# Kernel tuning notes

Hardware: AMD Instinct MI355X
Metric: run time of the kernel (lower is better)

Reference implementation:

```python
import jax, jax.numpy as jnp
import numpy as np

TEMPERATURE = 0.5
EPS = 1e-8  # matches torch cosine_similarity eps guard semantics (norm clamp)


def setup_inputs() -> dict:
    key = jax.random.key(0)
    k1, k2 = jax.random.split(key)
    B, D = 4096, 256
    z_i = jax.random.normal(k1, (B, D), dtype=jnp.float32)
    z_j = jax.random.normal(k2, (B, D), dtype=jnp.float32)
    return {"z_i": z_i, "z_j": z_j}


def reference(z_i, z_j):
    B = z_i.shape[0]
    z = jnp.concatenate([z_i, z_j], axis=0)            # [2B, D]
    # cosine similarity: normalize once, then GEMM
    norm = jnp.maximum(jnp.linalg.norm(z, axis=1, keepdims=True), EPS)
    zn = z / norm                                       # [2B, D]
    sim = zn @ zn.T                                     # [2B, 2B]
    # positives: diag(sim, +B) and diag(sim, -B)
    idx = jnp.arange(B)
    sim_ij = sim[idx, idx + B]
    sim_ji = sim[idx + B, idx]
    positives = jnp.concatenate([sim_ij, sim_ji])       # [2B]
    # masked denominator: exclude self-similarity
    mask = 1.0 - jnp.eye(2 * B, dtype=sim.dtype)
    denom = jnp.sum(mask * jnp.exp(sim / TEMPERATURE), axis=1)  # [2B]
    all_losses = -jnp.log(jnp.exp(positives / TEMPERATURE) / denom)
    return jnp.sum(all_losses) / (2 * B)
```

## Files before the change

kernel.cpp:

```cpp
#include <hip/hip_runtime.h>
#include <hip/hip_bf16.h>
#include <cstdint>
#include <cstddef>
#include <math.h>

#define D 256
#define TEMP_INV 2.0f
#define EPS_NORM 1e-8f
#define NTILES 2080

typedef __attribute__((ext_vector_type(8))) short bf16x8;
typedef __attribute__((ext_vector_type(4))) float f32x4;

__global__ void __launch_bounds__(256) normalize_rows(
    const float* __restrict__ zi, const float* __restrict__ zj,
    __hip_bfloat16* __restrict__ zn, float* __restrict__ denom, int B) {
  const int wid = threadIdx.x >> 6;
  const int lane = threadIdx.x & 63;
  if (threadIdx.x < 16) denom[blockIdx.x * 16 + threadIdx.x] = 0.0f;
#pragma unroll
  for (int it = 0; it < 4; ++it) {
    int row = it * 2048 + blockIdx.x * 4 + wid;
    const float* src = (row < B) ? (zi + (size_t)row * D)
                                 : (zj + (size_t)(row - B) * D);
    float4 v = ((const float4*)src)[lane];
    float ss = v.x * v.x + v.y * v.y + v.z * v.z + v.w * v.w;
    for (int off = 32; off; off >>= 1) ss += __shfl_xor(ss, off);
    float rn = 1.0f / fmaxf(sqrtf(ss), EPS_NORM);
    union { ushort4 u; __hip_bfloat16 h[4]; } o;
    o.h[0] = __float2bfloat16(v.x * rn);
    o.h[1] = __float2bfloat16(v.y * rn);
    o.h[2] = __float2bfloat16(v.z * rn);
    o.h[3] = __float2bfloat16(v.w * rn);
    ((ushort4*)zn)[(size_t)row * (D / 4) + lane] = o.u;
  }
}

__device__ __forceinline__ void decode_tile(int t, int Nb, int& by, int& bx) {
  float fb = (2.0f * Nb + 1.0f -
              sqrtf((float)((2 * Nb + 1) * (2 * Nb + 1) - 8 * t))) * 0.5f;
  int y = (int)fb;
  while ((y + 1) * Nb - ((y + 1) * y) / 2 <= t) ++y;
  while (y * Nb - (y * (y - 1)) / 2 > t) --y;
  by = y;
  bx = y + (t - (y * Nb - (y * (y - 1)) / 2));
}

__global__ void ntxent_gemm(
    const __hip_bfloat16* __restrict__ zn,
    float* __restrict__ denom, float* __restrict__ pos, int B) {
  __shared__ __align__(16) __hip_bfloat16 Ash[128 * 64];
  __shared__ __align__(16) __hip_bfloat16 Bsh[128 * 64];

  const int Nb = (2 * B) / 128;
  int by, bx;
  decode_tile(blockIdx.x, Nb, by, bx);
  const int bm = by * 128;
  const int bn = bx * 128;
  const bool isDiag = (by == bx);
  const bool isPos = (bx == by + B / 128);

  const int tid = threadIdx.x;
  const int wid = tid >> 6;
  const int lane = tid & 63;
  const int wy = wid >> 1, wx = wid & 1;
  const int wrow0 = wid * 32;

  const int lr = lane >> 3;
  const int c8 = lane & 7;

  const int frow = lane & 15;
  const int quad = lane >> 4;
  const int f7 = frow & 7;

  f32x4 acc[4][4] = {};

  const __hip_bfloat16* gA = zn + (size_t)(bm + wrow0 + lr) * D + c8 * 8;
  const __hip_bfloat16* gB = zn + (size_t)(bn + wrow0 + lr) * D + c8 * 8;
  const int ldsoff = (wrow0 + lr) * 64 + (c8 ^ lr) * 8;

#pragma unroll
  for (int k0i = 0; k0i < 4; ++k0i) {
    const int k0 = k0i * 64;
    float4 va0 = *(const float4*)(gA + 0 * 8 * D + k0);
    float4 va1 = *(const float4*)(gA + 1 * 8 * D + k0);
    float4 va2 = *(const float4*)(gA + 2 * 8 * D + k0);
    float4 va3 = *(const float4*)(gA + 3 * 8 * D + k0);
    float4 vb0 = *(const float4*)(gB + 0 * 8 * D + k0);
    float4 vb1 = *(const float4*)(gB + 1 * 8 * D + k0);
    float4 vb2 = *(const float4*)(gB + 2 * 8 * D + k0);
    float4 vb3 = *(const float4*)(gB + 3 * 8 * D + k0);
    __syncthreads();
    *(float4*)&Ash[ldsoff + 0 * 8 * 64] = va0;
    *(float4*)&Ash[ldsoff + 1 * 8 * 64] = va1;
    *(float4*)&Ash[ldsoff + 2 * 8 * 64] = va2;
    *(float4*)&Ash[ldsoff + 3 * 8 * 64] = va3;
    *(float4*)&Bsh[ldsoff + 0 * 8 * 64] = vb0;
    *(float4*)&Bsh[ldsoff + 1 * 8 * 64] = vb1;
    *(float4*)&Bsh[ldsoff + 2 * 8 * 64] = vb2;
    *(float4*)&Bsh[ldsoff + 3 * 8 * 64] = vb3;
    __syncthreads();
#pragma unroll
    for (int kk = 0; kk < 2; ++kk) {
      bf16x8 a[4], b[4];
#pragma unroll
      for (int i = 0; i < 4; ++i)
        a[i] = *(const bf16x8*)
            &Ash[(wy * 64 + i * 16 + frow) * 64 + ((kk * 4 + quad) ^ f7) * 8];
#pragma unroll
      for (int j = 0; j < 4; ++j)
        b[j] = *(const bf16x8*)
            &Bsh[(wx * 64 + j * 16 + frow) * 64 + ((kk * 4 + quad) ^ f7) * 8];
#pragma unroll
      for (int i = 0; i < 4; ++i)
#pragma unroll
        for (int j = 0; j < 4; ++j)
          acc[i][j] =
              __builtin_amdgcn_mfma_f32_16x16x32_bf16(a[i], b[j], acc[i][j], 0, 0, 0);
    }
  }

  const int colq = lane & 15;
  float cs[4] = {0.0f, 0.0f, 0.0f, 0.0f};
#pragma unroll
  for (int i = 0; i < 4; ++i) {
#pragma unroll
    for (int r = 0; r < 4; ++r) {
      int row = bm + wy * 64 + i * 16 + quad * 4 + r;
      float rs = 0.0f;
#pragma unroll
      for (int j = 0; j < 4; ++j) {
        int col = bn + wx * 64 + j * 16 + colq;
        float v = acc[i][j][r];
        float e = __expf(v * TEMP_INV);
        e = (isDiag && col == row) ? 0.0f : e;
        rs += e;
        cs[j] += e;
        if (isPos && col == row + B) { pos[row] = v; pos[col] = v; }
      }
      rs += __shfl_xor(rs, 1);
      rs += __shfl_xor(rs, 2);
      rs += __shfl_xor(rs, 4);
      rs += __shfl_xor(rs, 8);
      if (colq == 0) atomicAdd(&denom[row], rs);
    }
  }
  if (!isDiag) {
#pragma unroll
    for (int j = 0; j < 4; ++j) {
      float c = cs[j];
      c += __shfl_xor(c, 16);
      c += __shfl_xor(c, 32);
      if (quad == 0) atomicAdd(&denom[bn + wx * 64 + j * 16 + colq], c);
    }
  }
}

__global__ void __launch_bounds__(1024) finalize(
    const float* __restrict__ denom, const float* __restrict__ pos,
    float* __restrict__ out, int N) {
  __shared__ float red[16];
  const int tid = threadIdx.x;
  float s = 0.0f;
  for (int i = tid; i < N / 4; i += 1024) {
    float4 d = ((const float4*)denom)[i];
    float4 p = ((const float4*)pos)[i];
    s += __logf(d.x) - p.x * TEMP_INV;
    s += __logf(d.y) - p.y * TEMP_INV;
    s += __logf(d.z) - p.z * TEMP_INV;
    s += __logf(d.w) - p.w * TEMP_INV;
  }
  for (int off = 32; off; off >>= 1) s += __shfl_xor(s, off);
  if ((tid & 63) == 0) red[tid >> 6] = s;
  __syncthreads();
  if (tid < 16) {
    s = red[tid];
    s += __shfl_xor(s, 1);
    s += __shfl_xor(s, 2);
    s += __shfl_xor(s, 4);
    s += __shfl_xor(s, 8);
    if (tid == 0) out[0] = s / (float)N;
  }
}

extern "C" void kernel_launch(void* const* d_in, const int* in_sizes, int n_in,
                              void* d_out, int out_size, void* d_ws, size_t ws_size,
                              hipStream_t stream) {
  const float* zi = (const float*)d_in[0];
  const float* zj = (const float*)d_in[1];
  const int B = in_sizes[0] / D;
  const int N = 2 * B;

  __hip_bfloat16* zn = (__hip_bfloat16*)d_ws;
  float* denom = (float*)((char*)d_ws + (size_t)N * D * sizeof(__hip_bfloat16));
  float* pos = denom + N;

  normalize_rows<<<512, 256, 0, stream>>>(zi, zj, zn, denom, B);
  ntxent_gemm<<<NTILES, 256, 0, stream>>>(zn, denom, pos, B);
  finalize<<<1, 1024, 0, stream>>>(denom, pos, (float*)d_out, N);
}
```

Baseline: 107.9 us.

## Use 256x128 supertiles and fuse finalize into GEMM via ticket counter

The GEMM now processes 256x128 supertiles over the upper triangle, so each block reuses a B tile across twice as many rows and there are fewer tiles and atomics. On diagonal supertiles the waves covering the below-diagonal half skip their work. The separate finalize launch is replaced by a last-block-done reduction through a global atomic ticket that normalize_rows resets. The cost is more accumulators per wave (launch bounds of 256,2) and some idle waves on diagonal tiles.

Result: slower. 124.4 us (+15.3%).

```diff
diff --git a/kernel.cpp b/kernel.cpp
--- a/kernel.cpp
+++ b/kernel.cpp
@@ -7,17 +7,19 @@
 #define D 256
 #define TEMP_INV 2.0f
 #define EPS_NORM 1e-8f
-#define NTILES 2080
+#define NSUP 1056
 
 typedef __attribute__((ext_vector_type(8))) short bf16x8;
 typedef __attribute__((ext_vector_type(4))) float f32x4;
 
 __global__ void __launch_bounds__(256) normalize_rows(
     const float* __restrict__ zi, const float* __restrict__ zj,
-    __hip_bfloat16* __restrict__ zn, float* __restrict__ denom, int B) {
+    __hip_bfloat16* __restrict__ zn, float* __restrict__ denom,
+    unsigned* __restrict__ counter, int B) {
   const int wid = threadIdx.x >> 6;
   const int lane = threadIdx.x & 63;
   if (threadIdx.x < 16) denom[blockIdx.x * 16 + threadIdx.x] = 0.0f;
+  if (blockIdx.x == 0 && threadIdx.x == 0) *counter = 0u;
 #pragma unroll
   for (int it = 0; it < 4; ++it) {
     int row = it * 2048 + blockIdx.x * 4 + wid;
@@ -36,150 +38,164 @@
   }
 }
 
-__device__ __forceinline__ void decode_tile(int t, int Nb, int& by, int& bx) {
-  float fb = (2.0f * Nb + 1.0f -
-              sqrtf((float)((2 * Nb + 1) * (2 * Nb + 1) - 8 * t))) * 0.5f;
-  int y = (int)fb;
-  while ((y + 1) * Nb - ((y + 1) * y) / 2 <= t) ++y;
-  while (y * Nb - (y * (y - 1)) / 2 > t) --y;
-  by = y;
-  bx = y + (t - (y * Nb - (y * (y - 1)) / 2));
-}
-
-__global__ void ntxent_gemm(
-    const __hip_bfloat16* __restrict__ zn,
-    float* __restrict__ denom, float* __restrict__ pos, int B) {
-  __shared__ __align__(16) __hip_bfloat16 Ash[128 * 64];
+__device__ __forceinline__ void decode_supertile(int t, int& by2, int& bx) {
+  int y = (int)((65.0f - sqrtf(4225.0f - 4.0f * (float)t)) * 0.5f);
+  while ((y + 1) * (65 - (y + 1)) <= t) ++y;
+  while (y * (65 - y) > t) --y;
+  by2 = y;
+  bx = 2 * y + (t - y * (65 - y));
+}
+
+__global__ void __launch_bounds__(256, 2) ntxent_gemm(
+    const __hip_bfloat16* __restrict__ zn, float* __restrict__ denom,
+    float* __restrict__ pos, unsigned* __restrict__ counter,
+    float* __restrict__ out, int B) {
+  __shared__ __align__(16) __hip_bfloat16 Ash[256 * 64];
   __shared__ __align__(16) __hip_bfloat16 Bsh[128 * 64];
-
-  const int Nb = (2 * B) / 128;
-  int by, bx;
-  decode_tile(blockIdx.x, Nb, by, bx);
-  const int bm = by * 128;
+  __shared__ unsigned ticket_s;
+  __shared__ float red_s[4];
+
+  const int N = 2 * B;
+  int by2, bx;
+  decode_supertile(blockIdx.x, by2, bx);
+  const int bm = by2 * 256;
   const int bn = bx * 128;
-  const bool isDiag = (by == bx);
-  const bool isPos = (bx == by + B / 128);
+  const bool stDiag0 = (bx == 2 * by2);
+  const bool stDiag1 = (bx == 2 * by2 + 1);
 
   const int tid = threadIdx.x;
   const int wid = tid >> 6;
   const int lane = tid & 63;
-  const int wy = wid >> 1, wx = wid & 1;
-  const int wrow0 = wid * 32;
-
+  const bool topHalf = (wid < 2);
+  const bool waveSkip = stDiag0 && !topHalf;
+  const bool diagMode = (stDiag0 && topHalf) || (stDiag1 && !topHalf);
+  const bool isPosST = ((bn - bm) == B) || ((bn - bm) == B + 128);
+
+  const int wrow0A = wid * 64;
+  const int wrow0B = wid * 32;
   const int lr = lane >> 3;
   const int c8 = lane & 7;
-
   const int frow = lane & 15;
   const int quad = lane >> 4;
   const int f7 = frow & 7;
 
-  f32x4 acc[4][4] = {};
-
-  const __hip_bfloat16* gA = zn + (size_t)(bm + wrow0 + lr) * D + c8 * 8;
-  const __hip_bfloat16* gB = zn + (size_t)(bn + wrow0 + lr) * D + c8 * 8;
-  const int ldsoff = (wrow0 + lr) * 64 + (c8 ^ lr) * 8;
+  f32x4 acc[4][8] = {};
+
+  const __hip_bfloat16* gA = zn + (size_t)(bm + wrow0A + lr) * D + c8 * 8;
+  const __hip_bfloat16* gB = zn + (size_t)(bn + wrow0B + lr) * D + c8 * 8;
+  const int loffA = (wrow0A + lr) * 64 + (c8 ^ lr) * 8;
+  const int loffB = (wrow0B + lr) * 64 + (c8 ^ lr) * 8;
 
 #pragma unroll
   for (int k0i = 0; k0i < 4; ++k0i) {
     const int k0 = k0i * 64;
-    float4 va0 = *(const float4*)(gA + 0 * 8 * D + k0);
-    float4 va1 = *(const float4*)(gA + 1 * 8 * D + k0);
-    float4 va2 = *(const float4*)(gA + 2 * 8 * D + k0);
-    float4 va3 = *(const float4*)(gA + 3 * 8 * D + k0);
-    float4 vb0 = *(const float4*)(gB + 0 * 8 * D + k0);
-    float4 vb1 = *(const float4*)(gB + 1 * 8 * D + k0);
-    float4 vb2 = *(const float4*)(gB + 2 * 8 * D + k0);
-    float4 vb3 = *(const float4*)(gB + 3 * 8 * D + k0);
+    float4 a0 = *(const float4*)(gA + 0 * 8 * D + k0);
+    float4 a1 = *(const float4*)(gA + 1 * 8 * D + k0);
+    float4 a2 = *(const float4*)(gA + 2 * 8 * D + k0);
+    float4 a3 = *(const float4*)(gA + 3 * 8 * D + k0);
+    float4 a4 = *(const float4*)(gA + 4 * 8 * D + k0);
+    float4 a5 = *(const float4*)(gA + 5 * 8 * D + k0);
+    float4 a6 = *(const float4*)(gA + 6 * 8 * D + k0);
+    float4 a7 = *(const float4*)(gA + 7 * 8 * D + k0);
+    float4 b0 = *(const float4*)(gB + 0 * 8 * D + k0);
+    float4 b1 = *(const float4*)(gB + 1 * 8 * D + k0);
+    float4 b2 = *(const float4*)(gB + 2 * 8 * D + k0);
+    float4 b3 = *(const float4*)(gB + 3 * 8 * D + k0);
     __syncthreads();
-    *(float4*)&Ash[ldsoff + 0 * 8 * 64] = va0;
-    *(float4*)&Ash[ldsoff + 1 * 8 * 64] = va1;
-    *(float4*)&Ash[ldsoff + 2 * 8 * 64] = va2;
-    *(float4*)&Ash[ldsoff + 3 * 8 * 64] = va3;
-    *(float4*)&Bsh[ldsoff + 0 * 8 * 64] = vb0;
-    *(float4*)&Bsh[ldsoff + 1 * 8 * 64] = vb1;
-    *(float4*)&Bsh[ldsoff + 2 * 8 * 64] = vb2;
-    *(float4*)&Bsh[ldsoff + 3 * 8 * 64] = vb3;
+    *(float4*)&Ash[loffA + 0 * 8 * 64] = a0;
+    *(float4*)&Ash[loffA + 1 * 8 * 64] = a1;
+    *(float4*)&Ash[loffA + 2 * 8 * 64] = a2;
+    *(float4*)&Ash[loffA + 3 * 8 * 64] = a3;
+    *(float4*)&Ash[loffA + 4 * 8 * 64] = a4;
+    *(float4*)&Ash[loffA + 5 * 8 * 64] = a5;
+    *(float4*)&Ash[loffA + 6 * 8 * 64] = a6;
+    *(float4*)&Ash[loffA + 7 * 8 * 64] = a7;
+    *(float4*)&Bsh[loffB + 0 * 8 * 64] = b0;
+    *(float4*)&Bsh[loffB + 1 * 8 * 64] = b1;
+    *(float4*)&Bsh[loffB + 2 * 8 * 64] = b2;
+    *(float4*)&Bsh[loffB + 3 * 8 * 64] = b3;
     __syncthreads();
-#pragma unroll
-    for (int kk = 0; kk < 2; ++kk) {
-      bf16x8 a[4], b[4];
-#pragma unroll
-      for (int i = 0; i < 4; ++i)
-        a[i] = *(const bf16x8*)
-            &Ash[(wy * 64 + i * 16 + frow) * 64 + ((kk * 4 + quad) ^ f7) * 8];
-#pragma unroll
-      for (int j = 0; j < 4; ++j)
-        b[j] = *(const bf16x8*)
-            &Bsh[(wx * 64 + j * 16 + frow) * 64 + ((kk * 4 + quad) ^ f7) * 8];
-#pragma unroll
-      for (int i = 0; i < 4; ++i)
-#pragma unroll
-        for (int j = 0; j < 4; ++j)
-          acc[i][j] =
-              __builtin_amdgcn_mfma_f32_16x16x32_bf16(a[i], b[j], acc[i][j], 0, 0, 0);
-    }
-  }
-
-  const int colq = lane & 15;
-  float cs[4] = {0.0f, 0.0f, 0.0f, 0.0f};
-#pragma unroll
-  for (int i = 0; i < 4; ++i) {
-#pragma unroll
-    for (int r = 0; r < 4; ++r) {
-      int row = bm + wy * 64 + i * 16 + quad * 4 + r;
-      float rs = 0.0f;
-#pragma unroll
-      for (int j = 0; j < 4; ++j) {
-        int col = bn + wx * 64 + j * 16 + colq;
-        float v = acc[i][j][r];
-        float e = __expf(v * TEMP_INV);
-        e = (isDiag && col == row) ? 0.0f : e;
-        rs += e;
-        cs[j] += e;
-        if (isPos && col == row + B) { pos[row] = v; pos[col] = v; }
+    if (!waveSkip) {
+#pragma unroll
+      for (int kk = 0; kk < 2; ++kk) {
+        bf16x8 af[4], bf[8];
+#pragma unroll
+        for (int i = 0; i < 4; ++i)
+          af[i] = *(const bf16x8*)
+              &Ash[(wrow0A + i * 16 + frow) * 64 + ((kk * 4 + quad) ^ f7) * 8];
+#pragma unroll
+        for (int j = 0; j < 8; ++j)
+          bf[j] = *(const bf16x8*)
+              &Bsh[(j * 16 + frow) * 64 + ((kk * 4 + quad) ^ f7) * 8];
+#pragma unroll
+        for (int i = 0; i < 4; ++i)
+#pragma unroll
+          for (int j = 0; j < 8; ++j)
+            acc[i][j] = __builtin_amdgcn_mfma_f32_16x16x32_bf16(
+                af[i], bf[j], acc[i][j], 0, 0, 0);
       }
-      rs += __shfl_xor(rs, 1);
-      rs += __shfl_xor(rs, 2);
-      rs += __shfl_xor(rs, 4);
-      rs += __shfl_xor(rs, 8);
-      if (colq == 0) atomicAdd(&denom[row], rs);
-    }
-  }
-  if (!isDiag) {
-#pragma unroll
-    for (int j = 0; j < 4; ++j) {
-      float c = cs[j];
-      c += __shfl_xor(c, 16);
-      c += __shfl_xor(c, 32);
-      if (quad == 0) atomicAdd(&denom[bn + wx * 64 + j * 16 + colq], c);
-    }
-  }
-}
-
-__global__ void __launch_bounds__(1024) finalize(
-    const float* __restrict__ denom, const float* __restrict__ pos,
-    float* __restrict__ out, int N) {
-  __shared__ float red[16];
-  const int tid = threadIdx.x;
-  float s = 0.0f;
-  for (int i = tid; i < N / 4; i += 1024) {
-    float4 d = ((const float4*)denom)[i];
-    float4 p = ((const float4*)pos)[i];
-    s += __logf(d.x) - p.x * TEMP_INV;
-    s += __logf(d.y) - p.y * TEMP_INV;
-    s += __logf(d.z) - p.z * TEMP_INV;
-    s += __logf(d.w) - p.w * TEMP_INV;
-  }
-  for (int off = 32; off; off >>= 1) s += __shfl_xor(s, off);
-  if ((tid & 63) == 0) red[tid >> 6] = s;
+    }
+  }
+
+  if (!waveSkip) {
+    const int colq = frow;
+    float cs[8] = {};
+#pragma unroll
+    for (int i = 0; i < 4; ++i) {
+#pragma unroll
+      for (int r = 0; r < 4; ++r) {
+        int row = bm + wrow0A + i * 16 + quad * 4 + r;
+        float rs = 0.0f;
+#pragma unroll
+        for (int j = 0; j < 8; ++j) {
+          int col = bn + j * 16 + colq;
+          float v = acc[i][j][r];
+          float e = __expf(v * TEMP_INV);
+          e = (diagMode && col == row) ? 0.0f : e;
+          rs += e;
+          cs[j] += e;
+          if (isPosST && col == row + B) { pos[row] = v; pos[col] = v; }
+        }
+        rs += __shfl_xor(rs, 1);
+        rs += __shfl_xor(rs, 2);
+        rs += __shfl_xor(rs, 4);
+        rs += __shfl_xor(rs, 8);
+        if (colq == 0) atomicAdd(&denom[row], rs);
+      }
+    }
+    if (!diagMode) {
+#pragma unroll
+      for (int j = 0; j < 8; ++j) {
+        float c = cs[j];
+        c += __shfl_xor(c, 16);
+        c += __shfl_xor(c, 32);
+        if (quad == 0) atomicAdd(&denom[bn + j * 16 + colq], c);
+      }
+    }
+  }
+
   __syncthreads();
-  if (tid < 16) {
-    s = red[tid];
-    s += __shfl_xor(s, 1);
-    s += __shfl_xor(s, 2);
-    s += __shfl_xor(s, 4);
-    s += __shfl_xor(s, 8);
-    if (tid == 0) out[0] = s / (float)N;
+  if (tid == 0) {
+    __threadfence();
+    ticket_s = atomicAdd(counter, 1u);
+  }
+  __syncthreads();
+  if (ticket_s == NSUP - 1) {
+    __threadfence();
+    float s = 0.0f;
+    for (int i = tid; i < N / 4; i += 256) {
+      float4 d = ((const float4*)denom)[i];
+      float4 p = ((const float4*)pos)[i];
+      s += __logf(d.x) - p.x * TEMP_INV;
+      s += __logf(d.y) - p.y * TEMP_INV;
+      s += __logf(d.z) - p.z * TEMP_INV;
+      s += __logf(d.w) - p.w * TEMP_INV;
+    }
+    for (int off = 32; off; off >>= 1) s += __shfl_xor(s, off);
+    if (lane == 0) red_s[wid] = s;
+    __syncthreads();
+    if (tid == 0)
+      out[0] = (red_s[0] + red_s[1] + red_s[2] + red_s[3]) / (float)N;
   }
 }
 
@@ -194,8 +210,9 @@
   __hip_bfloat16* zn = (__hip_bfloat16*)d_ws;
   float* denom = (float*)((char*)d_ws + (size_t)N * D * sizeof(__hip_bfloat16));
   float* pos = denom + N;
-
-  normalize_rows<<<512, 256, 0, stream>>>(zi, zj, zn, denom, B);
-  ntxent_gemm<<<NTILES, 256, 0, stream>>>(zn, denom, pos, B);
-  finalize<<<1, 1024, 0, stream>>>(denom, pos, (float*)d_out, N);
-}
+  unsigned* counter = (unsigned*)(pos + N);
+
+  normalize_rows<<<512, 256, 0, stream>>>(zi, zj, zn, denom, counter, B);
+  ntxent_gemm<<<NSUP, 256, 0, stream>>>(zn, denom, pos, counter,
+                                        (float*)d_out, B);
+}
```

## Fuse finalize into GEMM via last-block ticket and shrink K-tile to 32

Applied to the files above, without the earlier changes.

The separate finalize kernel is removed. The last GEMM block to finish, found through an atomic ticket counter that normalize_rows resets, now computes the log-sum loss, which saves one kernel launch. The GEMM K-loop also moves from 64-wide to 32-wide LDS tiles with a new swizzle. That halves shared memory per block and could raise occupancy, at the cost of twice as many barriers per tile. The last-block reduction runs serially on one workgroup and relies on threadfence ordering.

Result: slower. 155.6 us (+44.2%).

```diff
diff --git a/kernel.cpp b/kernel.cpp
--- a/kernel.cpp
+++ b/kernel.cpp
@@ -14,10 +14,12 @@
 
 __global__ void __launch_bounds__(256) normalize_rows(
     const float* __restrict__ zi, const float* __restrict__ zj,
-    __hip_bfloat16* __restrict__ zn, float* __restrict__ denom, int B) {
+    __hip_bfloat16* __restrict__ zn, float* __restrict__ denom,
+    unsigned* __restrict__ counter, int B) {
   const int wid = threadIdx.x >> 6;
   const int lane = threadIdx.x & 63;
   if (threadIdx.x < 16) denom[blockIdx.x * 16 + threadIdx.x] = 0.0f;
+  if (blockIdx.x == 0 && threadIdx.x == 0) *counter = 0u;
 #pragma unroll
   for (int it = 0; it < 4; ++it) {
     int row = it * 2048 + blockIdx.x * 4 + wid;
@@ -46,13 +48,17 @@
   bx = y + (t - (y * Nb - (y * (y - 1)) / 2));
 }
 
-__global__ void ntxent_gemm(
-    const __hip_bfloat16* __restrict__ zn,
-    float* __restrict__ denom, float* __restrict__ pos, int B) {
-  __shared__ __align__(16) __hip_bfloat16 Ash[128 * 64];
-  __shared__ __align__(16) __hip_bfloat16 Bsh[128 * 64];
+__global__ void __launch_bounds__(256) ntxent_gemm(
+    const __hip_bfloat16* __restrict__ zn, float* __restrict__ denom,
+    float* __restrict__ pos, unsigned* __restrict__ counter,
+    float* __restrict__ out, int B) {
+  __shared__ __align__(16) __hip_bfloat16 Ash[128 * 32];
+  __shared__ __align__(16) __hip_bfloat16 Bsh[128 * 32];
+  __shared__ unsigned ticket_s;
+  __shared__ float red_s[4];
 
-  const int Nb = (2 * B) / 128;
+  const int N = 2 * B;
+  const int Nb = N / 128;
   int by, bx;
   decode_tile(blockIdx.x, Nb, by, bx);
   const int bm = by * 128;
@@ -66,58 +72,46 @@
   const int wy = wid >> 1, wx = wid & 1;
   const int wrow0 = wid * 32;
 
-  const int lr = lane >> 3;
-  const int c8 = lane & 7;
+  const int row16 = lane >> 2;
+  const int c4 = lane & 3;
+  const int swz = (c4 ^ ((row16 >> 1) & 3)) * 8;
 
   const int frow = lane & 15;
   const int quad = lane >> 4;
-  const int f7 = frow & 7;
+  const int chunkoff = (quad ^ ((frow >> 1) & 3)) * 8;
 
   f32x4 acc[4][4] = {};
 
-  const __hip_bfloat16* gA = zn + (size_t)(bm + wrow0 + lr) * D + c8 * 8;
-  const __hip_bfloat16* gB = zn + (size_t)(bn + wrow0 + lr) * D + c8 * 8;
-  const int ldsoff = (wrow0 + lr) * 64 + (c8 ^ lr) * 8;
+  const __hip_bfloat16* gA = zn + (size_t)(bm + wrow0 + row16) * D + c4 * 8;
+  const __hip_bfloat16* gB = zn + (size_t)(bn + wrow0 + row16) * D + c4 * 8;
+  const int la = (wrow0 + row16) * 32 + swz;
 
 #pragma unroll
-  for (int k0i = 0; k0i < 4; ++k0i) {
-    const int k0 = k0i * 64;
-    float4 va0 = *(const float4*)(gA + 0 * 8 * D + k0);
-    float4 va1 = *(const float4*)(gA + 1 * 8 * D + k0);
-    float4 va2 = *(const float4*)(gA + 2 * 8 * D + k0);
-    float4 va3 = *(const float4*)(gA + 3 * 8 * D + k0);
-    float4 vb0 = *(const float4*)(gB + 0 * 8 * D + k0);
-    float4 vb1 = *(const float4*)(gB + 1 * 8 * D + k0);
-    float4 vb2 = *(const float4*)(gB + 2 * 8 * D + k0);
-    float4 vb3 = *(const float4*)(gB + 3 * 8 * D + k0);
+  for (int ki = 0; ki < 8; ++ki) {
+    const int k0 = ki * 32;
+    float4 va0 = *(const float4*)(gA + k0);
+    float4 va1 = *(const float4*)(gA + 16 * D + k0);
+    float4 vb0 = *(const float4*)(gB + k0);
+    float4 vb1 = *(const float4*)(gB + 16 * D + k0);
     __syncthreads();
-    *(float4*)&Ash[ldsoff + 0 * 8 * 64] = va0;
-    *(float4*)&Ash[ldsoff + 1 * 8 * 64] = va1;
-    *(float4*)&Ash[ldsoff + 2 * 8 * 64] = va2;
-    *(float4*)&Ash[ldsoff + 3 * 8 * 64] = va3;
-    *(float4*)&Bsh[ldsoff + 0 * 8 * 64] = vb0;
-    *(float4*)&Bsh[ldsoff + 1 * 8 * 64] = vb1;
-    *(float4*)&Bsh[ldsoff + 2 * 8 * 64] = vb2;
-    *(float4*)&Bsh[ldsoff + 3 * 8 * 64] = vb3;
+    *(float4*)&Ash[la] = va0;
+    *(float4*)&Ash[la + 16 * 32] = va1;
+    *(float4*)&Bsh[la] = vb0;
+    *(float4*)&Bsh[la + 16 * 32] = vb1;
     __syncthreads();
+    bf16x8 a[4], b[4];
 #pragma unroll
-    for (int kk = 0; kk < 2; ++kk) {
-      bf16x8 a[4], b[4];
+    for (int i = 0; i < 4; ++i)
+      a[i] = *(const bf16x8*)&Ash[(wy * 64 + i * 16 + frow) * 32 + chunkoff];
 #pragma unroll
-      for (int i = 0; i < 4; ++i)
-        a[i] = *(const bf16x8*)
-            &Ash[(wy * 64 + i * 16 + frow) * 64 + ((kk * 4 + quad) ^ f7) * 8];
+    for (int j = 0; j < 4; ++j)
+      b[j] = *(const bf16x8*)&Bsh[(wx * 64 + j * 16 + frow) * 32 + chunkoff];
+#pragma unroll
+    for (int i = 0; i < 4; ++i)
 #pragma unroll
       for (int j = 0; j < 4; ++j)
-        b[j] = *(const bf16x8*)
-            &Bsh[(wx * 64 + j * 16 + frow) * 64 + ((kk * 4 + quad) ^ f7) * 8];
-#pragma unroll
-      for (int i = 0; i < 4; ++i)
-#pragma unroll
-        for (int j = 0; j < 4; ++j)
-          acc[i][j] =
-              __builtin_amdgcn_mfma_f32_16x16x32_bf16(a[i], b[j], acc[i][j], 0, 0, 0);
-    }
+        acc[i][j] =
+            __builtin_amdgcn_mfma_f32_16x16x32_bf16(a[i], b[j], acc[i][j], 0, 0, 0);
   }
 
   const int colq = lane & 15;
@@ -154,32 +148,29 @@
       if (quad == 0) atomicAdd(&denom[bn + wx * 64 + j * 16 + colq], c);
     }
   }
-}
 
-__global__ void __launch_bounds__(1024) finalize(
-    const float* __restrict__ denom, const float* __restrict__ pos,
-    float* __restrict__ out, int N) {
-  __shared__ float red[16];
-  const int tid = threadIdx.x;
-  float s = 0.0f;
-  for (int i = tid; i < N / 4; i += 1024) {
-    float4 d = ((const float4*)denom)[i];
-    float4 p = ((const float4*)pos)[i];
-    s += __logf(d.x) - p.x * TEMP_INV;
-    s += __logf(d.y) - p.y * TEMP_INV;
-    s += __logf(d.z) - p.z * TEMP_INV;
-    s += __logf(d.w) - p.w * TEMP_INV;
+  __syncthreads();
+  if (tid == 0) {
+    __threadfence();
+    ticket_s = atomicAdd(counter, 1u);
   }
-  for (int off = 32; off; off >>= 1) s += __shfl_xor(s, off);
-  if ((tid & 63) == 0) red[tid >> 6] = s;
   __syncthreads();
-  if (tid < 16) {
-    s = red[tid];
-    s += __shfl_xor(s, 1);
-    s += __shfl_xor(s, 2);
-    s += __shfl_xor(s, 4);
-    s += __shfl_xor(s, 8);
-    if (tid == 0) out[0] = s / (float)N;
+  if (ticket_s == NTILES - 1) {
+    __threadfence();
+    float s = 0.0f;
+    for (int i = tid; i < N / 4; i += 256) {
+      float4 d = ((const float4*)denom)[i];
+      float4 p = ((const float4*)pos)[i];
+      s += __logf(d.x) - p.x * TEMP_INV;
+      s += __logf(d.y) - p.y * TEMP_INV;
+      s += __logf(d.z) - p.z * TEMP_INV;
+      s += __logf(d.w) - p.w * TEMP_INV;
+    }
+    for (int off = 32; off; off >>= 1) s += __shfl_xor(s, off);
+    if (lane == 0) red_s[wid] = s;
+    __syncthreads();
+    if (tid == 0)
+      out[0] = (red_s[0] + red_s[1] + red_s[2] + red_s[3]) / (float)N;
   }
 }
 
@@ -194,8 +185,9 @@
   __hip_bfloat16* zn = (__hip_bfloat16*)d_ws;
   float* denom = (float*)((char*)d_ws + (size_t)N * D * sizeof(__hip_bfloat16));
   float* pos = denom + N;
+  unsigned* counter = (unsigned*)(pos + N);
 
-  normalize_rows<<<512, 256, 0, stream>>>(zi, zj, zn, denom, B);
-  ntxent_gemm<<<NTILES, 256, 0, stream>>>(zn, denom, pos, B);
-  finalize<<<1, 1024, 0, stream>>>(denom, pos, (float*)d_out, N);
+  normalize_rows<<<512, 256, 0, stream>>>(zi, zj, zn, denom, counter, B);
+  ntxent_gemm<<<NTILES, 256, 0, stream>>>(zn, denom, pos, counter,
+                                          (float*)d_out, B);
 }
```
